# Performance work log

Hardware: AMD Instinct MI355X
Metric: run time of the kernel (lower is better)

Reference implementation:

```python
import jax, jax.numpy as jnp
import numpy as np
from jax import lax
from functools import partial

NPOINT = 2048
RADIUS = 1.0
NSAMPLE = 32


def _fps(xyz, npoint):
    # Farthest point sampling, sequential as in the classic CUDA kernel.
    # xyz: (N, 3) -> (npoint,) int32 indices; starts at index 0.
    N = xyz.shape[0]
    init_d = jnp.full((N,), jnp.inf, dtype=xyz.dtype)

    def step(carry, _):
        dists, last = carry
        delta = xyz - xyz[last]                      # (N, 3)
        nd = jnp.sum(delta * delta, axis=-1)         # (N,)
        dists = jnp.minimum(dists, nd)
        nxt = jnp.argmax(dists).astype(jnp.int32)
        return (dists, nxt), last

    (_, _), idxs = lax.scan(step, (init_d, jnp.int32(0)), None, length=npoint)
    return idxs


def _ball_query(radius, nsample, xyz, new_xyz):
    # xyz: (N, 3), new_xyz: (S, 3) -> (S, nsample) int32.
    # Take the first nsample points (in original order) within radius of each
    # centroid; pad with the first found index (centroid itself always hits).
    N = xyz.shape[0]
    d2 = (jnp.sum(new_xyz * new_xyz, -1, keepdims=True)
          + jnp.sum(xyz * xyz, -1)[None, :]
          - 2.0 * new_xyz @ xyz.T)                   # (S, N)
    mask = d2 < radius * radius
    key = jnp.where(mask, jnp.arange(N, dtype=jnp.int32), jnp.int32(N))  # (S, N)
    neg_topk, _ = lax.top_k(-key, nsample)           # nsample smallest keys
    idx = -neg_topk                                  # (S, nsample), ascending
    first = idx[:, :1]
    return jnp.where(idx == N, first, idx)


def setup_inputs() -> dict:
    key = jax.random.key(0)
    inputs = jax.random.normal(key, (4, 8192, 16), dtype=jnp.float32)
    return {"inputs": inputs}


def reference(inputs):
    xyz = inputs[..., :3]                            # (B, N, 3)
    points = inputs[..., 3:]                         # (B, N, C)

    fps_idx = jax.vmap(lambda p: _fps(p, NPOINT))(xyz)          # (B, S)
    new_xyz = jnp.take_along_axis(xyz, fps_idx[..., None], axis=1)  # (B, S, 3)

    idx = jax.vmap(partial(_ball_query, RADIUS, NSAMPLE))(xyz, new_xyz)  # (B, S, K)

    gather = jax.vmap(lambda p, i: p[i])             # (N, C), (S, K) -> (S, K, C)
    grouped_xyz = gather(xyz, idx) - new_xyz[:, :, None, :]      # (B, S, K, 3)
    grouped_points = gather(points, idx)                         # (B, S, K, C)
    new_points = jnp.concatenate([grouped_xyz, grouped_points], axis=-1)
    return new_xyz, new_points, idx, grouped_xyz
```

## Files before the change

### kernel.cpp

```cpp
#include <hip/hip_runtime.h>

#pragma clang fp contract(off)

#define NPOINT 2048
#define NSAMPLE 32
#define NPTS 8192
#define NB 4
#define CH 16
#define FPS_THREADS 1024
#define PTS_PER_THREAD (NPTS / FPS_THREADS)
#define PAIRS (PTS_PER_THREAD / 2)
#define FPS_WAVES (FPS_THREADS / 64)

typedef unsigned long long u64;
typedef float v2f __attribute__((ext_vector_type(2)));

#define OFF_NEWXYZ 0
#define OFF_NEWPTS (NB * NPOINT * 3)
#define OFF_IDX (OFF_NEWPTS + NB * NPOINT * NSAMPLE * CH)
#define OFF_GXYZ (OFF_IDX + NB * NPOINT * NSAMPLE)

template <int CTRL>
__device__ __forceinline__ float dpp_fmax(float v) {
  int o = __builtin_amdgcn_update_dpp(0, __float_as_int(v), CTRL, 0xf, 0xf, true);
  return fmaxf(v, __int_as_float(o));
}

__global__ __launch_bounds__(FPS_THREADS)
__attribute__((amdgpu_waves_per_eu(4, 4))) void fps_kernel(
    const float* __restrict__ in, float* __restrict__ out) {
  __shared__ float4 lpxyz[NPTS];
  __shared__ float newb[NPOINT * 3];
  __shared__ u64 slots[2][FPS_WAVES];

  const int b = blockIdx.x;
  const int tid = threadIdx.x;
  const int lane = tid & 63;
  const int wv = tid >> 6;
  const float* base = in + (size_t)b * NPTS * CH;

  v2f pxv[PAIRS], pyv[PAIRS], pzv[PAIRS], dv[PAIRS];
#pragma unroll
  for (int jp = 0; jp < PAIRS; ++jp) {
    int p0 = tid * PTS_PER_THREAD + 2 * jp;
    float4 r0 = *reinterpret_cast<const float4*>(base + (size_t)p0 * CH);
    float4 r1 = *reinterpret_cast<const float4*>(base + (size_t)(p0 + 1) * CH);
    pxv[jp] = (v2f){r0.x, r1.x};
    pyv[jp] = (v2f){r0.y, r1.y};
    pzv[jp] = (v2f){r0.z, r1.z};
    lpxyz[p0] = r0;
    lpxyz[p0 + 1] = r1;
    dv[jp] = (v2f){__builtin_inff(), __builtin_inff()};
  }
  if (tid < FPS_WAVES)
    slots[0][tid] = (tid == 0) ? (u64)0x7f800000u : (u64)0xbf800000u;

  for (int it = 0; it < NPOINT; ++it) {
    const int pb = it & 1;
    __syncthreads();
    u64 sl = slots[pb][lane & 15];
    float sd = __int_as_float((int)(unsigned)sl);
    int sidx = (int)(unsigned)(sl >> 32);
    float m = sd;
    m = dpp_fmax<0x111>(m);
    m = dpp_fmax<0x112>(m);
    m = dpp_fmax<0x114>(m);
    m = dpp_fmax<0x118>(m);
    const float smax =
        __int_as_float(__builtin_amdgcn_readlane(__float_as_int(m), 15));
    const u64 bal = __ballot(sd == smax) & 0xFFFFull;
    const int wwin = (int)__builtin_ctzll(bal);
    const int gi = __builtin_amdgcn_readlane(sidx, wwin);
    float4 g = lpxyz[gi];
    const float gx = g.x, gy = g.y, gz = g.z;
    if (tid == 0) {
      newb[it * 3 + 0] = gx;
      newb[it * 3 + 1] = gy;
      newb[it * 3 + 2] = gz;
    }
    float bestv = -1.0f;
#pragma unroll
    for (int jp = 0; jp < PAIRS; ++jp) {
      v2f dx = pxv[jp] - gx;
      v2f dy = pyv[jp] - gy;
      v2f dz = pzv[jp] - gz;
      v2f nd = (dx * dx + dy * dy) + dz * dz;
      v2f dn = {fminf(dv[jp].x, nd.x), fminf(dv[jp].y, nd.y)};
      dv[jp] = dn;
      bestv = fmaxf(bestv, fmaxf(dn.x, dn.y));
    }
    const float* df = (const float*)dv;
    int bestj = 0;
#pragma unroll
    for (int jj = PTS_PER_THREAD - 1; jj >= 0; --jj)
      if (df[jj] == bestv) bestj = jj;
    const int besti = tid * PTS_PER_THREAD + bestj;
    float wm = bestv;
    wm = dpp_fmax<0x111>(wm);
    wm = dpp_fmax<0x112>(wm);
    wm = dpp_fmax<0x114>(wm);
    wm = dpp_fmax<0x118>(wm);
    wm = dpp_fmax<0x142>(wm);
    wm = dpp_fmax<0x143>(wm);
    const float swm =
        __int_as_float(__builtin_amdgcn_readlane(__float_as_int(wm), 63));
    const u64 wbal = __ballot(bestv == swm);
    const int wl = (int)__builtin_ctzll(wbal);
    const int widx = __builtin_amdgcn_readlane(besti, wl);
    if (lane == 0)
      slots[pb ^ 1][wv] =
          ((u64)(unsigned)widx << 32) | (unsigned)__float_as_int(swm);
  }
  __syncthreads();
  float* ob = out + OFF_NEWXYZ + (size_t)b * NPOINT * 3;
  for (int i = tid; i < NPOINT * 3; i += FPS_THREADS) ob[i] = newb[i];
}

__device__ __forceinline__ void write_slot(float* __restrict__ out,
                                           const float* __restrict__ base,
                                           int b, int qi, int s, int p,
                                           float4 r0, float qx, float qy,
                                           float qz) {
  float dx = __fsub_rn(r0.x, qx);
  float dy = __fsub_rn(r0.y, qy);
  float dz = __fsub_rn(r0.z, qz);
  size_t qs = (size_t)b * NPOINT + qi;
  out[OFF_IDX + qs * NSAMPLE + s] = (float)p;
  float* g = out + OFF_GXYZ + (qs * NSAMPLE + s) * 3;
  g[0] = dx;
  g[1] = dy;
  g[2] = dz;
  const float* row = base + (size_t)p * CH;
  float4 r1 = *reinterpret_cast<const float4*>(row + 4);
  float4 r2 = *reinterpret_cast<const float4*>(row + 8);
  float4 r3 = *reinterpret_cast<const float4*>(row + 12);
  float* np_ = out + OFF_NEWPTS + (qs * NSAMPLE + s) * CH;
  *reinterpret_cast<float4*>(np_ + 0) = make_float4(dx, dy, dz, r0.w);
  *reinterpret_cast<float4*>(np_ + 4) = r1;
  *reinterpret_cast<float4*>(np_ + 8) = r2;
  *reinterpret_cast<float4*>(np_ + 12) = r3;
}

__global__ __launch_bounds__(256) void ballq_kernel(
    const float* __restrict__ in, float* __restrict__ out) {
  const int lane = threadIdx.x & 63;
  const int qid = blockIdx.x * 4 + (threadIdx.x >> 6);
  const int b = qid >> 11;
  const int qi = qid & 2047;
  const float* base = in + (size_t)b * NPTS * CH;
  const float* q = out + OFF_NEWXYZ + ((size_t)b * NPOINT + qi) * 3;
  float qx = q[0], qy = q[1], qz = q[2];
  float qn = __fadd_rn(__fadd_rn(__fmul_rn(qx, qx), __fmul_rn(qy, qy)),
                       __fmul_rn(qz, qz));

  int cnt = 0;
  int first = 0;
  bool have_first = false;
  for (int chunk = 0; chunk < NPTS / 64 && cnt < NSAMPLE; ++chunk) {
    int p = chunk * 64 + lane;
    float4 r0 = *reinterpret_cast<const float4*>(base + (size_t)p * CH);
    float pn =
        __fadd_rn(__fadd_rn(__fmul_rn(r0.x, r0.x), __fmul_rn(r0.y, r0.y)),
                  __fmul_rn(r0.z, r0.z));
    float dot =
        __fadd_rn(__fadd_rn(__fmul_rn(qx, r0.x), __fmul_rn(qy, r0.y)),
                  __fmul_rn(qz, r0.z));
    float d2 = __fsub_rn(__fadd_rn(qn, pn), __fmul_rn(2.0f, dot));
    bool in_r = d2 < 1.0f;
    unsigned long long mask = __ballot(in_r);
    if (!have_first && mask) {
      first = chunk * 64 + __builtin_ctzll(mask);
      have_first = true;
    }
    int pos = cnt + __popcll(mask & ((1ull << lane) - 1ull));
    if (in_r && pos < NSAMPLE) write_slot(out, base, b, qi, pos, p, r0, qx, qy, qz);
    cnt += __popcll(mask);
  }
  if (cnt < NSAMPLE) {
    int s = cnt + lane;
    if (s < NSAMPLE) {
      float4 r0 = *reinterpret_cast<const float4*>(base + (size_t)first * CH);
      write_slot(out, base, b, qi, s, first, r0, qx, qy, qz);
    }
  }
}

extern "C" void kernel_launch(void* const* d_in, const int* in_sizes, int n_in,
                              void* d_out, int out_size, void* d_ws,
                              size_t ws_size, hipStream_t stream) {
  (void)in_sizes;
  (void)n_in;
  (void)out_size;
  (void)d_ws;
  (void)ws_size;
  const float* in = (const float*)d_in[0];
  float* out = (float*)d_out;
  fps_kernel<<<NB, FPS_THREADS, 0, stream>>>(in, out);
  ballq_kernel<<<(NB * NPOINT) / 4, 256, 0, stream>>>(in, out);
}
```

Measured before the change: 2.029 ms.

## Replace per-wave slot reduction in FPS with LDS 64-bit atomicMax key

FPS now uses 512 threads with 16 points per thread instead of 1024 with 8. The cross-wave argmax no longer writes per-wave slots that every wave re-reduces with DPP. Instead, each wave's winning lanes do a 64-bit LDS atomicMax on a packed (distance, inverted index) key, and three rotating slots allow one barrier per iteration. This cuts the post-barrier reduction latency on the serial critical path. In exchange it adds LDS atomic contention and doubles per-thread register work.

Result: slower. 2.093 ms (+3.2%).

```diff
diff --git a/kernel.cpp b/kernel.cpp
--- a/kernel.cpp
+++ b/kernel.cpp
@@ -7,10 +7,9 @@
 #define NPTS 8192
 #define NB 4
 #define CH 16
-#define FPS_THREADS 1024
+#define FPS_THREADS 512
 #define PTS_PER_THREAD (NPTS / FPS_THREADS)
 #define PAIRS (PTS_PER_THREAD / 2)
-#define FPS_WAVES (FPS_THREADS / 64)
 
 typedef unsigned long long u64;
 typedef float v2f __attribute__((ext_vector_type(2)));
@@ -27,16 +26,14 @@
 }
 
 __global__ __launch_bounds__(FPS_THREADS)
-__attribute__((amdgpu_waves_per_eu(4, 4))) void fps_kernel(
+__attribute__((amdgpu_waves_per_eu(2))) void fps_kernel(
     const float* __restrict__ in, float* __restrict__ out) {
   __shared__ float4 lpxyz[NPTS];
   __shared__ float newb[NPOINT * 3];
-  __shared__ u64 slots[2][FPS_WAVES];
+  __shared__ u64 kslot[3];
 
   const int b = blockIdx.x;
   const int tid = threadIdx.x;
-  const int lane = tid & 63;
-  const int wv = tid >> 6;
   const float* base = in + (size_t)b * NPTS * CH;
 
   v2f pxv[PAIRS], pyv[PAIRS], pzv[PAIRS], dv[PAIRS];
@@ -52,28 +49,21 @@
     lpxyz[p0 + 1] = r1;
     dv[jp] = (v2f){__builtin_inff(), __builtin_inff()};
   }
-  if (tid < FPS_WAVES)
-    slots[0][tid] = (tid == 0) ? (u64)0x7f800000u : (u64)0xbf800000u;
+  if (tid == 0) {
+    kslot[0] = ((u64)0x7f800000u << 32) | 8191u;
+    kslot[1] = 0;
+    kslot[2] = 0;
+  }
 
+  int rd = 0, at = 1, rs = 2;
   for (int it = 0; it < NPOINT; ++it) {
-    const int pb = it & 1;
     __syncthreads();
-    u64 sl = slots[pb][lane & 15];
-    float sd = __int_as_float((int)(unsigned)sl);
-    int sidx = (int)(unsigned)(sl >> 32);
-    float m = sd;
-    m = dpp_fmax<0x111>(m);
-    m = dpp_fmax<0x112>(m);
-    m = dpp_fmax<0x114>(m);
-    m = dpp_fmax<0x118>(m);
-    const float smax =
-        __int_as_float(__builtin_amdgcn_readlane(__float_as_int(m), 15));
-    const u64 bal = __ballot(sd == smax) & 0xFFFFull;
-    const int wwin = (int)__builtin_ctzll(bal);
-    const int gi = __builtin_amdgcn_readlane(sidx, wwin);
-    float4 g = lpxyz[gi];
+    const u64 k = kslot[rd];
+    const int gi = 8191 - (int)(unsigned)k;
+    const float4 g = lpxyz[gi];
     const float gx = g.x, gy = g.y, gz = g.z;
     if (tid == 0) {
+      kslot[rs] = 0;
       newb[it * 3 + 0] = gx;
       newb[it * 3 + 1] = gy;
       newb[it * 3 + 2] = gz;
@@ -87,7 +77,7 @@
       v2f nd = (dx * dx + dy * dy) + dz * dz;
       v2f dn = {fminf(dv[jp].x, nd.x), fminf(dv[jp].y, nd.y)};
       dv[jp] = dn;
-      bestv = fmaxf(bestv, fmaxf(dn.x, dn.y));
+      bestv = fmaxf(fmaxf(bestv, dn.x), dn.y);
     }
     const float* df = (const float*)dv;
     int bestj = 0;
@@ -104,12 +94,14 @@
     wm = dpp_fmax<0x143>(wm);
     const float swm =
         __int_as_float(__builtin_amdgcn_readlane(__float_as_int(wm), 63));
-    const u64 wbal = __ballot(bestv == swm);
-    const int wl = (int)__builtin_ctzll(wbal);
-    const int widx = __builtin_amdgcn_readlane(besti, wl);
-    if (lane == 0)
-      slots[pb ^ 1][wv] =
-          ((u64)(unsigned)widx << 32) | (unsigned)__float_as_int(swm);
+    if (bestv == swm) {
+      u64 key = ((u64)__float_as_uint(bestv) << 32) | (8191u - (unsigned)besti);
+      atomicMax(&kslot[at], key);
+    }
+    const int t = rd;
+    rd = at;
+    at = rs;
+    rs = t;
   }
   __syncthreads();
   float* ob = out + OFF_NEWXYZ + (size_t)b * NPOINT * 3;
```
